# Performance work log

Hardware: AMD Instinct MI355X
Metric: run time of the kernel (lower is better)

The kernel has to match this reference:

```python
import jax, jax.numpy as jnp
import numpy as np

DIM = 2048        # model hidden size
INTER = 1408      # per-expert intermediate size
E = 16            # n_routed_experts
TOPK = 2          # n_activated_experts
S_INTER = 2816    # shared experts intermediate (n_shared_experts * INTER)
T = 4096          # tokens (batch*seq, module flattens to [-1, dim])
ROUTE_SCALE = 1.0


def setup_inputs() -> dict:
    key = jax.random.key(0)
    ks = jax.random.split(key, 8)
    g = lambda k, shape, scale: (jax.random.normal(k, shape, dtype=jnp.float32) * scale)
    return {
        "x": g(ks[0], (T, DIM), 1.0),
        "gate_w": g(ks[1], (E, DIM), 0.02),
        "w1": g(ks[2], (E, INTER, DIM), 0.02),
        "w2": g(ks[3], (E, DIM, INTER), 0.02),
        "w3": g(ks[4], (E, INTER, DIM), 0.02),
        "sw1": g(ks[5], (S_INTER, DIM), 0.02),
        "sw2": g(ks[6], (DIM, S_INTER), 0.02),
        "sw3": g(ks[7], (S_INTER, DIM), 0.02),
    }


def _moe_forward(x, gate_w, w1, w2, w3, sw1, sw2, sw3):
    t = x.shape[0]
    # ---- gate: softmax scores -> top-k experts per token ----
    scores = jax.nn.softmax(x @ gate_w.T, axis=-1)          # [T, E]
    top_w, top_i = jax.lax.top_k(scores, TOPK)              # [T, K]
    top_w = top_w * ROUTE_SCALE
    # dense combine weights [T, E]: zero for unselected experts
    combine = jnp.zeros((t, E), x.dtype).at[jnp.arange(t)[:, None], top_i].add(top_w)
    # ---- routed experts: gated silu MLP per expert, weighted combine ----
    # loop over the small fixed expert count; tokens with combine==0 contribute 0,
    # matching the original scatter/gather dispatch math exactly.
    y = jnp.zeros_like(x)
    for e in range(E):
        h = jax.nn.silu(x @ w1[e].T) * (x @ w3[e].T)        # [T, INTER]
        y = y + (h @ w2[e].T) * combine[:, e:e + 1]
    # ---- shared experts ----
    z = (jax.nn.silu(x @ sw1.T) * (x @ sw3.T)) @ sw2.T      # [T, DIM]
    return y + z


def reference(x, gate_w, w1, w2, w3, sw1, sw2, sw3):
    return _moe_forward(x, gate_w, w1, w2, w3, sw1, sw2, sw3)
```

## Files before the change

### kernel.cpp

```cpp
#include <hip/hip_runtime.h>
#include <hip/hip_bf16.h>
#include <cstdint>
#include <cstddef>

#define TTOK   4096
#define DIM_   2048
#define INTER_ 1408
#define NEXP   16
#define SINTER_ 2816
#define BM 128
#define BN 128
#define BK 64
#define MAXROWS (TTOK*2 + NEXP*BM)
#define MAXMT   (TTOK*2/BM + NEXP)

typedef unsigned short u16;
typedef __attribute__((ext_vector_type(8))) short short8;
typedef __attribute__((ext_vector_type(4))) float f32x4;

#define AS3P(p) ((__attribute__((address_space(3))) void*)(p))
#define AS1P(p) ((const __attribute__((address_space(1))) void*)(p))

__device__ __forceinline__ void gll16(const void* g, void* l) {
    __builtin_amdgcn_global_load_lds(AS1P(g), AS3P(l), 16, 0, 0);
}

__device__ __forceinline__ u16 f2bf(float f) {
    __hip_bfloat16 h = __float2bfloat16(f);
    union { __hip_bfloat16 h; u16 u; } c; c.h = h; return c.u;
}

__device__ __forceinline__ unsigned pk2(float a, float b) {
    unsigned r;
    asm("v_cvt_pk_bf16_f32 %0, %1, %2" : "=v"(r) : "v"(a), "v"(b));
    return r;
}

__device__ __forceinline__ int4 pack8(float4 a, float4 b) {
    int4 r;
    r.x = (int)pk2(a.x, a.y);
    r.y = (int)pk2(a.z, a.w);
    r.z = (int)pk2(b.x, b.y);
    r.w = (int)pk2(b.z, b.w);
    return r;
}


__global__ void init_kernel(int* perm_rt, float* pw_rt, int* misc, int* zrow) {
    int i = blockIdx.x * 256 + threadIdx.x;
    if (i < MAXROWS) { perm_rt[i] = -1; pw_rt[i] = 0.f; }
    if (i < 32)      misc[i] = 0;
    if (i < 1024)    zrow[i] = 0;
}

#define NW8  ((long)NEXP * INTER_ * DIM_ / 8)
#define NSW8 ((long)SINTER_ * DIM_ / 8)
#define NX8  ((long)TTOK * DIM_ / 8)
#define TOT8 (3 * NW8 + 3 * NSW8 + NX8)

__global__ void cvt_all_kernel(
    const float* __restrict__ w1, const float* __restrict__ w2,
    const float* __restrict__ w3, const float* __restrict__ sw1,
    const float* __restrict__ sw2, const float* __restrict__ sw3,
    const float* __restrict__ x,
    u16* __restrict__ w1b, u16* __restrict__ w2b, u16* __restrict__ w3b,
    u16* __restrict__ sw1b, u16* __restrict__ sw2b, u16* __restrict__ sw3b,
    u16* __restrict__ xb)
{
    const long stride = (long)gridDim.x * 256;
    for (long i = (long)blockIdx.x * 256 + threadIdx.x; i < TOT8; i += stride) {
        const float* s; u16* d; long off;
        if      (i <     NW8)              { s = w1;  d = w1b;  off = i; }
        else if (i < 2 * NW8)              { s = w2;  d = w2b;  off = i - NW8; }
        else if (i < 3 * NW8)              { s = w3;  d = w3b;  off = i - 2 * NW8; }
        else if (i < 3 * NW8 + NSW8)       { s = sw1; d = sw1b; off = i - 3 * NW8; }
        else if (i < 3 * NW8 + 2 * NSW8)   { s = sw2; d = sw2b; off = i - 3 * NW8 - NSW8; }
        else if (i < 3 * NW8 + 3 * NSW8)   { s = sw3; d = sw3b; off = i - 3 * NW8 - 2 * NSW8; }
        else                               { s = x;   d = xb;   off = i - 3 * NW8 - 3 * NSW8; }
        const float4* s4 = (const float4*)(s + off * 8);
        float4 a = s4[0], b = s4[1];
        *(int4*)(d + off * 8) = pack8(a, b);
    }
}

__global__ void gate_kernel(const float* __restrict__ x, const float* __restrict__ gw,
                            int* __restrict__ topi, float* __restrict__ topw,
                            int* __restrict__ misc) {
    int t = blockIdx.x;
    int lane = threadIdx.x;
    const float* xr = x + (size_t)t * DIM_;
    float acc[NEXP];
#pragma unroll
    for (int e = 0; e < NEXP; e++) acc[e] = 0.f;
#pragma unroll
    for (int i = 0; i < 8; i++) {
        int k = i * 256 + lane * 4;
        float4 xv = *(const float4*)(xr + k);
#pragma unroll
        for (int e = 0; e < NEXP; e++) {
            float4 gv = *(const float4*)(gw + (size_t)e * DIM_ + k);
            acc[e] += xv.x * gv.x + xv.y * gv.y + xv.z * gv.z + xv.w * gv.w;
        }
    }
#pragma unroll
    for (int e = 0; e < NEXP; e++) {
        float v = acc[e];
        for (int off = 32; off > 0; off >>= 1) v += __shfl_down(v, off);
        acc[e] = v;
    }
    if (lane == 0) {
        float m = acc[0];
#pragma unroll
        for (int e = 1; e < NEXP; e++) m = fmaxf(m, acc[e]);
        float p[NEXP]; float s = 0.f;
#pragma unroll
        for (int e = 0; e < NEXP; e++) { p[e] = __expf(acc[e] - m); s += p[e]; }
        int i0 = 0; float v0 = p[0];
#pragma unroll
        for (int e = 1; e < NEXP; e++) if (p[e] > v0) { v0 = p[e]; i0 = e; }
        int i1 = -1; float v1 = -1.f;
#pragma unroll
        for (int e = 0; e < NEXP; e++) if (e != i0 && p[e] > v1) { v1 = p[e]; i1 = e; }
        float inv = 1.f / s;
        topi[2 * t] = i0; topi[2 * t + 1] = i1;
        topw[2 * t] = v0 * inv; topw[2 * t + 1] = v1 * inv;
        atomicAdd(&misc[i0], 1);
        atomicAdd(&misc[i1], 1);
    }
}

__global__ void scan_kernel(int* misc) {
    int* counts = misc;
    int* base   = misc + 32;
    int* te     = misc + 48;
    int* tr     = misc + 128;
    int b = 0, tt = 0;
    for (int e = 0; e < NEXP; e++) {
        int c = counts[e];
        int nt = (c + BM - 1) >> 7;
        base[e] = b;
        for (int i = 0; i < nt; i++) { te[tt] = e; tr[tt] = b + i * BM; tt++; }
        b += nt * BM;
    }
    for (int i = tt; i < MAXMT; i++) te[i] = -1;
}

__global__ void scatter_kernel(const int* __restrict__ topi, const float* __restrict__ topw,
                               int* __restrict__ misc, int* __restrict__ perm,
                               float* __restrict__ pw) {
    int t = blockIdx.x * 256 + threadIdx.x;
    if (t >= TTOK) return;
    int* fill = misc + 16;
    int* base = misc + 32;
#pragma unroll
    for (int k = 0; k < 2; k++) {
        int e = topi[2 * t + k];
        int pos = base[e] + atomicAdd(&fill[e], 1);
        perm[pos] = t;
        pw[pos] = topw[2 * t + k];
    }
}


template<bool GROUPED>
__global__ __launch_bounds__(256, 2) void gemm_h13_k(
    const u16* __restrict__ Xb,
    const u16* __restrict__ W1b, const u16* __restrict__ W3b,
    u16* __restrict__ H,
    const int* __restrict__ perm,
    const int* __restrict__ te, const int* __restrict__ tr,
    const u16* __restrict__ zrow,
    int N, int K, int nt_m, int chunk)
{
    const int q = (blockIdx.x & 7) * chunk + (blockIdx.x >> 3);
    if (q >= nt_m * (N / BN)) return;
    const int jn = q / nt_m, im = q % nt_m;
    int e, slot0;
    if (GROUPED) { e = te[im]; if (e < 0) return; slot0 = tr[im]; }
    else         { e = 0; slot0 = im * BM; }
    const int n0 = jn * BN;
    const u16* W1 = W1b + (size_t)e * N * K;
    const u16* W3 = W3b + (size_t)e * N * K;

    __shared__ __align__(16) u16 As[BM * BK];
    __shared__ __align__(16) u16 B1s[BM * BK];
    __shared__ __align__(16) u16 B3s[BM * BK];

    const int tid = threadIdx.x;
    const int lane = tid & 63, wid = tid >> 6;
    const int wr = wid >> 1, wc = wid & 1;
    const int col = lane & 15, kg = lane >> 4;

    const int lr8 = lane >> 3;
    const int kb  = ((lane & 7) ^ lr8) * 8;
    const int rB0 = wid * 32 + lr8;
    const u16* gA[4];
#pragma unroll
    for (int i = 0; i < 4; i++) {
        if (GROUPED) {
            int ta = perm[slot0 + rB0 + 8 * i];
            gA[i] = (ta >= 0 ? Xb + (size_t)ta * K : zrow) + kb;
        } else {
            gA[i] = Xb + (size_t)(slot0 + rB0 + 8 * i) * K + kb;
        }
    }
    const u16* g1 = W1 + (size_t)(n0 + rB0) * K + kb;
    const u16* g3 = W3 + (size_t)(n0 + rB0) * K + kb;

    const int ldsI = (wid * 32) * BK;
    const int swr = col & 7;

    f32x4 acc1[4][4] = {};
    f32x4 acc3[4][4] = {};

    for (int k0 = 0; k0 < K; k0 += BK) {
#pragma unroll
        for (int i = 0; i < 4; i++) {
            gll16(gA[i] + k0, As + ldsI + i * 8 * BK);
            gll16(g1 + (size_t)(8 * i) * K + k0, B1s + ldsI + i * 8 * BK);
            gll16(g3 + (size_t)(8 * i) * K + k0, B3s + ldsI + i * 8 * BK);
        }
        __syncthreads();

        short8 a[4][2];
#pragma unroll
        for (int mi = 0; mi < 4; mi++)
#pragma unroll
            for (int t = 0; t < 2; t++) {
                int cc = kg + 4 * t;
                a[mi][t] = *(const short8*)(As + (wr * 64 + mi * 16 + col) * BK + ((cc ^ swr) * 8));
            }
#pragma unroll
        for (int t = 0; t < 2; t++) {
#pragma unroll
            for (int ni = 0; ni < 4; ni++) {
                int cc = kg + 4 * t;
                int off = (wc * 64 + ni * 16 + col) * BK + ((cc ^ swr) * 8);
                short8 v1 = *(const short8*)(B1s + off);
                short8 v3 = *(const short8*)(B3s + off);
#pragma unroll
                for (int mi = 0; mi < 4; mi++) {
                    acc1[mi][ni] = __builtin_amdgcn_mfma_f32_16x16x32_bf16(a[mi][t], v1, acc1[mi][ni], 0, 0, 0);
                    acc3[mi][ni] = __builtin_amdgcn_mfma_f32_16x16x32_bf16(a[mi][t], v3, acc3[mi][ni], 0, 0, 0);
                }
            }
        }
        __syncthreads();
    }

#pragma unroll
    for (int mi = 0; mi < 4; mi++) {
#pragma unroll
        for (int j = 0; j < 4; j++) {
            int row = slot0 + wr * 64 + mi * 16 + kg * 4 + j;
#pragma unroll
            for (int ni = 0; ni < 4; ni++) {
                float v1 = acc1[mi][ni][j];
                float v3 = acc3[mi][ni][j];
                float hv = v1 / (1.f + __expf(-v1)) * v3;
                int c = n0 + wc * 64 + ni * 16 + col;
                H[(size_t)row * N + c] = f2bf(hv);
            }
        }
    }
}


template<bool ATOMIC>
__global__ __launch_bounds__(256, 3) void gemm_out_k(
    const u16* __restrict__ Hm,
    const u16* __restrict__ W2b,
    float* __restrict__ Out,
    const int* __restrict__ perm, const float* __restrict__ pw,
    const int* __restrict__ te, const int* __restrict__ tr,
    int K, int nt_m, int chunk)
{
    const int q = (blockIdx.x & 7) * chunk + (blockIdx.x >> 3);
    if (q >= nt_m * (DIM_ / BN)) return;
    const int jn = q / nt_m, im = q % nt_m;
    int e, slot0;
    if (ATOMIC) { e = te[im]; if (e < 0) return; slot0 = tr[im]; }
    else        { e = 0; slot0 = im * BM; }
    const int n0 = jn * BN;
    const u16* W2 = W2b + (size_t)e * DIM_ * K;

    __shared__ __align__(16) u16 As[BM * BK];
    __shared__ __align__(16) u16 Bs[BM * BK];

    const int tid = threadIdx.x;
    const int lane = tid & 63, wid = tid >> 6;
    const int wr = wid >> 1, wc = wid & 1;
    const int col = lane & 15, kg = lane >> 4;

    const int lr8 = lane >> 3;
    const int kb  = ((lane & 7) ^ lr8) * 8;
    const int rB0 = wid * 32 + lr8;
    const u16* gA = Hm + (size_t)(slot0 + rB0) * K + kb;
    const u16* gB = W2 + (size_t)(n0 + rB0) * K + kb;
    const int ldsI = (wid * 32) * BK;
    const int swr = col & 7;

    f32x4 acc[4][4] = {};

    for (int k0 = 0; k0 < K; k0 += BK) {
#pragma unroll
        for (int i = 0; i < 4; i++) {
            gll16(gA + (size_t)(8 * i) * K + k0, As + ldsI + i * 8 * BK);
            gll16(gB + (size_t)(8 * i) * K + k0, Bs + ldsI + i * 8 * BK);
        }
        __syncthreads();

        short8 a[4][2];
#pragma unroll
        for (int mi = 0; mi < 4; mi++)
#pragma unroll
            for (int t = 0; t < 2; t++) {
                int cc = kg + 4 * t;
                a[mi][t] = *(const short8*)(As + (wr * 64 + mi * 16 + col) * BK + ((cc ^ swr) * 8));
            }
#pragma unroll
        for (int t = 0; t < 2; t++) {
#pragma unroll
            for (int ni = 0; ni < 4; ni++) {
                int cc = kg + 4 * t;
                int off = (wc * 64 + ni * 16 + col) * BK + ((cc ^ swr) * 8);
                short8 bv = *(const short8*)(Bs + off);
#pragma unroll
                for (int mi = 0; mi < 4; mi++)
                    acc[mi][ni] = __builtin_amdgcn_mfma_f32_16x16x32_bf16(a[mi][t], bv, acc[mi][ni], 0, 0, 0);
            }
        }
        __syncthreads();
    }

#pragma unroll
    for (int mi = 0; mi < 4; mi++) {
#pragma unroll
        for (int j = 0; j < 4; j++) {
            int rloc = wr * 64 + mi * 16 + kg * 4 + j;
            int slot = slot0 + rloc;
            if (ATOMIC) {
                int token = perm[slot];
                if (token < 0) continue;
                float w = pw[slot];
#pragma unroll
                for (int ni = 0; ni < 4; ni++) {
                    int c = n0 + wc * 64 + ni * 16 + col;
                    atomicAdd(&Out[(size_t)token * DIM_ + c], acc[mi][ni][j] * w);
                }
            } else {
#pragma unroll
                for (int ni = 0; ni < 4; ni++) {
                    int c = n0 + wc * 64 + ni * 16 + col;
                    Out[(size_t)slot * DIM_ + c] = acc[mi][ni][j];
                }
            }
        }
    }
}


extern "C" void kernel_launch(void* const* d_in, const int* in_sizes, int n_in,
                              void* d_out, int out_size, void* d_ws, size_t ws_size,
                              hipStream_t stream) {
    (void)in_sizes; (void)n_in; (void)out_size; (void)ws_size;
    const float* x   = (const float*)d_in[0];
    const float* gw  = (const float*)d_in[1];
    const float* w1  = (const float*)d_in[2];
    const float* w2  = (const float*)d_in[3];
    const float* w3  = (const float*)d_in[4];
    const float* sw1 = (const float*)d_in[5];
    const float* sw2 = (const float*)d_in[6];
    const float* sw3 = (const float*)d_in[7];
    float* out = (float*)d_out;

    char* ws = (char*)d_ws;
    size_t off = 0;
    auto take = [&](size_t bytes) -> void* {
        void* p = ws + off;
        off += (bytes + 255) & ~(size_t)255;
        return p;
    };
    const size_t nHB = ((size_t)MAXROWS * INTER_ > (size_t)TTOK * SINTER_)
                       ? (size_t)MAXROWS * INTER_ : (size_t)TTOK * SINTER_;
    u16*   xb      = (u16*)take((size_t)TTOK * DIM_ * 2);
    u16*   hbuf    = (u16*)take(nHB * 2);
    int*   perm_rt = (int*)take((size_t)MAXROWS * 4);
    float* pw_rt   = (float*)take((size_t)MAXROWS * 4);
    int*   topi    = (int*)take((size_t)TTOK * 2 * 4);
    float* topw    = (float*)take((size_t)TTOK * 2 * 4);
    int*   misc    = (int*)take(1024);
    int*   zrow    = (int*)take(4096);
    const size_t nW  = (size_t)NEXP * INTER_ * DIM_;
    const size_t nSW = (size_t)SINTER_ * DIM_;
    u16* w1b  = (u16*)take(nW * 2);
    u16* w2b  = (u16*)take(nW * 2);
    u16* w3b  = (u16*)take(nW * 2);
    u16* sw1b = (u16*)take(nSW * 2);
    u16* sw2b = (u16*)take(nSW * 2);
    u16* sw3b = (u16*)take(nSW * 2);

    init_kernel<<<MAXROWS / 256, 256, 0, stream>>>(perm_rt, pw_rt, misc, zrow);
    cvt_all_kernel<<<4096, 256, 0, stream>>>(w1, w2, w3, sw1, sw2, sw3, x,
                                             w1b, w2b, w3b, sw1b, sw2b, sw3b, xb);
    gate_kernel<<<TTOK, 64, 0, stream>>>(x, gw, topi, topw, misc);
    scan_kernel<<<1, 1, 0, stream>>>(misc);
    scatter_kernel<<<TTOK / 256, 256, 0, stream>>>(topi, topw, misc, perm_rt, pw_rt);

    auto grid8 = [](int total) { return ((total + 7) / 8) * 8; };
    auto chunk8 = [](int total) { return (total + 7) / 8; };

    const int ntm_sh = TTOK / BM;

    {
        int total = ntm_sh * (SINTER_ / BN);
        gemm_h13_k<false><<<grid8(total), 256, 0, stream>>>(
            xb, sw1b, sw3b, hbuf, nullptr, nullptr, nullptr, (const u16*)zrow,
            SINTER_, DIM_, ntm_sh, chunk8(total));
    }
    {
        int total = ntm_sh * (DIM_ / BN);
        gemm_out_k<false><<<grid8(total), 256, 0, stream>>>(
            hbuf, sw2b, out, nullptr, nullptr, nullptr, nullptr,
            SINTER_, ntm_sh, chunk8(total));
    }
    {
        int total = MAXMT * (INTER_ / BN);
        gemm_h13_k<true><<<grid8(total), 256, 0, stream>>>(
            xb, w1b, w3b, hbuf, perm_rt, misc + 48, misc + 128, (const u16*)zrow,
            INTER_, DIM_, MAXMT, chunk8(total));
    }
    {
        int total = MAXMT * (DIM_ / BN);
        gemm_out_k<true><<<grid8(total), 256, 0, stream>>>(
            hbuf, w2b, out, perm_rt, pw_rt, misc + 48, misc + 128,
            INTER_, MAXMT, chunk8(total));
    }
}
```

Baseline: 818.8 us.

## Double-buffer LDS tiles with async prefetch in both MoE GEMM kernels

Replaces the single-buffer BK=64 load/sync/compute loop with two LDS buffers of K-depth 32, issuing global_load_lds for the tile two steps ahead and waiting with explicit vmcnt counts plus barriers. Global-to-LDS latency can then overlap with MFMA work instead of stalling at each __syncthreads. The swizzle is redone for 32-wide rows, and the down-projection kernel's occupancy hint rises from 3 to 4 blocks. Each step now does half the MFMA work per barrier, so barrier overhead per FLOP goes up, and the hand-written waitcnt values must match the number of loads in flight.

After: 875.1 us. 6.9% more time.

```diff
diff --git a/kernel.cpp b/kernel.cpp
--- a/kernel.cpp
+++ b/kernel.cpp
@@ -10,7 +10,7 @@
 #define SINTER_ 2816
 #define BM 128
 #define BN 128
-#define BK 64
+#define HK 32
 #define MAXROWS (TTOK*2 + NEXP*BM)
 #define MAXMT   (TTOK*2/BM + NEXP)
 
@@ -44,6 +44,17 @@
     r.w = (int)pk2(b.z, b.w);
     return r;
 }
+
+#define PWAIT(NLIT) do { \
+    asm volatile("s_waitcnt vmcnt(" #NLIT ")" ::: "memory"); \
+    __builtin_amdgcn_s_barrier(); \
+    asm volatile("" ::: "memory"); \
+} while (0)
+#define PDONE() do { \
+    asm volatile("" ::: "memory"); \
+    __builtin_amdgcn_s_barrier(); \
+    asm volatile("" ::: "memory"); \
+} while (0)
 
 
 __global__ void init_kernel(int* perm_rt, float* pw_rt, int* misc, int* zrow) {
@@ -182,70 +193,82 @@
     const u16* W1 = W1b + (size_t)e * N * K;
     const u16* W3 = W3b + (size_t)e * N * K;
 
-    __shared__ __align__(16) u16 As[BM * BK];
-    __shared__ __align__(16) u16 B1s[BM * BK];
-    __shared__ __align__(16) u16 B3s[BM * BK];
+    __shared__ __align__(16) u16 As[2][BM * HK];
+    __shared__ __align__(16) u16 B1s[2][BM * HK];
+    __shared__ __align__(16) u16 B3s[2][BM * HK];
 
     const int tid = threadIdx.x;
     const int lane = tid & 63, wid = tid >> 6;
     const int wr = wid >> 1, wc = wid & 1;
     const int col = lane & 15, kg = lane >> 4;
 
-    const int lr8 = lane >> 3;
-    const int kb  = ((lane & 7) ^ lr8) * 8;
-    const int rB0 = wid * 32 + lr8;
-    const u16* gA[4];
-#pragma unroll
-    for (int i = 0; i < 4; i++) {
-        if (GROUPED) {
-            int ta = perm[slot0 + rB0 + 8 * i];
-            gA[i] = (ta >= 0 ? Xb + (size_t)ta * K : zrow) + kb;
-        } else {
-            gA[i] = Xb + (size_t)(slot0 + rB0 + 8 * i) * K + kb;
-        }
-    }
-    const u16* g1 = W1 + (size_t)(n0 + rB0) * K + kb;
-    const u16* g3 = W3 + (size_t)(n0 + rB0) * K + kb;
-
-    const int ldsI = (wid * 32) * BK;
-    const int swr = col & 7;
+    const int lr = lane >> 2;
+    const int kb = ((lane & 3) ^ ((lane >> 3) & 3)) * 8;
+    const int ar0 = wid * 32 + lr, ar1 = ar0 + 16;
+    const u16* ga0;
+    const u16* ga1;
+    if (GROUPED) {
+        const int ta0 = perm[slot0 + ar0];
+        const int ta1 = perm[slot0 + ar1];
+        ga0 = (ta0 >= 0 ? Xb + (size_t)ta0 * K : zrow) + kb;
+        ga1 = (ta1 >= 0 ? Xb + (size_t)ta1 * K : zrow) + kb;
+    } else {
+        ga0 = Xb + (size_t)(slot0 + ar0) * K + kb;
+        ga1 = Xb + (size_t)(slot0 + ar1) * K + kb;
+    }
+    const u16* gb1a = W1 + (size_t)(n0 + ar0) * K + kb;
+    const u16* gb1b = W1 + (size_t)(n0 + ar1) * K + kb;
+    const u16* gb3a = W3 + (size_t)(n0 + ar0) * K + kb;
+    const u16* gb3b = W3 + (size_t)(n0 + ar1) * K + kb;
+    const int lo0 = (wid * 32) * HK;
+    const int lo1 = (wid * 32 + 16) * HK;
+
+    const int sw = (col >> 1) & 3;
 
     f32x4 acc1[4][4] = {};
     f32x4 acc3[4][4] = {};
 
-    for (int k0 = 0; k0 < K; k0 += BK) {
-#pragma unroll
-        for (int i = 0; i < 4; i++) {
-            gll16(gA[i] + k0, As + ldsI + i * 8 * BK);
-            gll16(g1 + (size_t)(8 * i) * K + k0, B1s + ldsI + i * 8 * BK);
-            gll16(g3 + (size_t)(8 * i) * K + k0, B3s + ldsI + i * 8 * BK);
-        }
-        __syncthreads();
-
-        short8 a[4][2];
+    auto ISSUE = [&](int h) {
+        const int b = h & 1;
+        const int ko = h * HK;
+        gll16(ga0 + ko, &As[b][lo0]);
+        gll16(ga1 + ko, &As[b][lo1]);
+        gll16(gb1a + ko, &B1s[b][lo0]);
+        gll16(gb1b + ko, &B1s[b][lo1]);
+        gll16(gb3a + ko, &B3s[b][lo0]);
+        gll16(gb3b + ko, &B3s[b][lo1]);
+    };
+
+    const int nh = K / HK;
+    ISSUE(0);
+    ISSUE(1);
+
+    for (int h = 0; h < nh; ++h) {
+        if (h + 1 < nh) PWAIT(6); else PWAIT(0);
+
+        const int b = h & 1;
+        const u16* Ac  = As[b];
+        const u16* B1c = B1s[b];
+        const u16* B3c = B3s[b];
+
+        short8 a[4];
 #pragma unroll
         for (int mi = 0; mi < 4; mi++)
-#pragma unroll
-            for (int t = 0; t < 2; t++) {
-                int cc = kg + 4 * t;
-                a[mi][t] = *(const short8*)(As + (wr * 64 + mi * 16 + col) * BK + ((cc ^ swr) * 8));
-            }
-#pragma unroll
-        for (int t = 0; t < 2; t++) {
-#pragma unroll
-            for (int ni = 0; ni < 4; ni++) {
-                int cc = kg + 4 * t;
-                int off = (wc * 64 + ni * 16 + col) * BK + ((cc ^ swr) * 8);
-                short8 v1 = *(const short8*)(B1s + off);
-                short8 v3 = *(const short8*)(B3s + off);
-#pragma unroll
-                for (int mi = 0; mi < 4; mi++) {
-                    acc1[mi][ni] = __builtin_amdgcn_mfma_f32_16x16x32_bf16(a[mi][t], v1, acc1[mi][ni], 0, 0, 0);
-                    acc3[mi][ni] = __builtin_amdgcn_mfma_f32_16x16x32_bf16(a[mi][t], v3, acc3[mi][ni], 0, 0, 0);
-                }
+            a[mi] = *(const short8*)(Ac + (wr * 64 + mi * 16 + col) * HK + ((kg ^ sw) * 8));
+#pragma unroll
+        for (int ni = 0; ni < 4; ni++) {
+            const int off = (wc * 64 + ni * 16 + col) * HK + ((kg ^ sw) * 8);
+            short8 v1 = *(const short8*)(B1c + off);
+            short8 v3 = *(const short8*)(B3c + off);
+#pragma unroll
+            for (int mi = 0; mi < 4; mi++) {
+                acc1[mi][ni] = __builtin_amdgcn_mfma_f32_16x16x32_bf16(a[mi], v1, acc1[mi][ni], 0, 0, 0);
+                acc3[mi][ni] = __builtin_amdgcn_mfma_f32_16x16x32_bf16(a[mi], v3, acc3[mi][ni], 0, 0, 0);
             }
         }
-        __syncthreads();
+
+        PDONE();
+        if (h + 2 < nh) ISSUE(h + 2);
     }
 
 #pragma unroll
@@ -267,7 +290,7 @@
 
 
 template<bool ATOMIC>
-__global__ __launch_bounds__(256, 3) void gemm_out_k(
+__global__ __launch_bounds__(256, 4) void gemm_out_k(
     const u16* __restrict__ Hm,
     const u16* __restrict__ W2b,
     float* __restrict__ Out,
@@ -284,53 +307,62 @@
     const int n0 = jn * BN;
     const u16* W2 = W2b + (size_t)e * DIM_ * K;
 
-    __shared__ __align__(16) u16 As[BM * BK];
-    __shared__ __align__(16) u16 Bs[BM * BK];
+    __shared__ __align__(16) u16 As[2][BM * HK];
+    __shared__ __align__(16) u16 Bs[2][BM * HK];
 
     const int tid = threadIdx.x;
     const int lane = tid & 63, wid = tid >> 6;
     const int wr = wid >> 1, wc = wid & 1;
     const int col = lane & 15, kg = lane >> 4;
 
-    const int lr8 = lane >> 3;
-    const int kb  = ((lane & 7) ^ lr8) * 8;
-    const int rB0 = wid * 32 + lr8;
-    const u16* gA = Hm + (size_t)(slot0 + rB0) * K + kb;
-    const u16* gB = W2 + (size_t)(n0 + rB0) * K + kb;
-    const int ldsI = (wid * 32) * BK;
-    const int swr = col & 7;
+    const int lr = lane >> 2;
+    const int kb = ((lane & 3) ^ ((lane >> 3) & 3)) * 8;
+    const int ar0 = wid * 32 + lr, ar1 = ar0 + 16;
+    const u16* ga0 = Hm + (size_t)(slot0 + ar0) * K + kb;
+    const u16* ga1 = Hm + (size_t)(slot0 + ar1) * K + kb;
+    const u16* gb0 = W2 + (size_t)(n0 + ar0) * K + kb;
+    const u16* gb1 = W2 + (size_t)(n0 + ar1) * K + kb;
+    const int lo0 = (wid * 32) * HK;
+    const int lo1 = (wid * 32 + 16) * HK;
+
+    const int sw = (col >> 1) & 3;
 
     f32x4 acc[4][4] = {};
 
-    for (int k0 = 0; k0 < K; k0 += BK) {
-#pragma unroll
-        for (int i = 0; i < 4; i++) {
-            gll16(gA + (size_t)(8 * i) * K + k0, As + ldsI + i * 8 * BK);
-            gll16(gB + (size_t)(8 * i) * K + k0, Bs + ldsI + i * 8 * BK);
+    auto ISSUE = [&](int h) {
+        const int b = h & 1;
+        const int ko = h * HK;
+        gll16(ga0 + ko, &As[b][lo0]);
+        gll16(ga1 + ko, &As[b][lo1]);
+        gll16(gb0 + ko, &Bs[b][lo0]);
+        gll16(gb1 + ko, &Bs[b][lo1]);
+    };
+
+    const int nh = K / HK;
+    ISSUE(0);
+    ISSUE(1);
+
+    for (int h = 0; h < nh; ++h) {
+        if (h + 1 < nh) PWAIT(4); else PWAIT(0);
+
+        const int b = h & 1;
+        const u16* Ac = As[b];
+        const u16* Bc = Bs[b];
+
+        short8 a[4];
+#pragma unroll
+        for (int mi = 0; mi < 4; mi++)
+            a[mi] = *(const short8*)(Ac + (wr * 64 + mi * 16 + col) * HK + ((kg ^ sw) * 8));
+#pragma unroll
+        for (int ni = 0; ni < 4; ni++) {
+            short8 bv = *(const short8*)(Bc + (wc * 64 + ni * 16 + col) * HK + ((kg ^ sw) * 8));
+#pragma unroll
+            for (int mi = 0; mi < 4; mi++)
+                acc[mi][ni] = __builtin_amdgcn_mfma_f32_16x16x32_bf16(a[mi], bv, acc[mi][ni], 0, 0, 0);
         }
-        __syncthreads();
-
-        short8 a[4][2];
-#pragma unroll
-        for (int mi = 0; mi < 4; mi++)
-#pragma unroll
-            for (int t = 0; t < 2; t++) {
-                int cc = kg + 4 * t;
-                a[mi][t] = *(const short8*)(As + (wr * 64 + mi * 16 + col) * BK + ((cc ^ swr) * 8));
-            }
-#pragma unroll
-        for (int t = 0; t < 2; t++) {
-#pragma unroll
-            for (int ni = 0; ni < 4; ni++) {
-                int cc = kg + 4 * t;
-                int off = (wc * 64 + ni * 16 + col) * BK + ((cc ^ swr) * 8);
-                short8 bv = *(const short8*)(Bs + off);
-#pragma unroll
-                for (int mi = 0; mi < 4; mi++)
-                    acc[mi][ni] = __builtin_amdgcn_mfma_f32_16x16x32_bf16(a[mi][t], bv, acc[mi][ni], 0, 0, 0);
-            }
-        }
-        __syncthreads();
+
+        PDONE();
+        if (h + 2 < nh) ISSUE(h + 2);
     }
 
 #pragma unroll
```

## Merge shared and routed expert GEMMs into single launches per stage

Applied to the files above, without the earlier changes.

Folds the shared-expert GEMMs into the routed-expert GEMM launches, so one kernel computes both H stages and one kernel computes both output projections. Shared weights are laid out right after the routed weights so a single base pointer plus offset addresses either. Output is zeroed inside the conversion kernel, which also absorbs the separate init kernel. Every output write now goes through an atomic add, and the larger grids are meant to fill the device better and cut launch gaps and tail effects. The cost is extra atomic traffic for the shared-expert outputs.

After: 818.8 us. No clear change (-0.0%).

```diff
diff --git a/kernel.cpp b/kernel.cpp
--- a/kernel.cpp
+++ b/kernel.cpp
@@ -14,6 +14,13 @@
 #define MAXROWS (TTOK*2 + NEXP*BM)
 #define MAXMT   (TTOK*2/BM + NEXP)
 
+#define NT_SH_H  ((TTOK/BM) * (SINTER_/BN))
+#define NT_RT_H  (MAXMT * (INTER_/BN))
+#define NT_H     (NT_SH_H + NT_RT_H)
+#define NT_SH_O  ((TTOK/BM) * (DIM_/BN))
+#define NT_RT_O  (MAXMT * (DIM_/BN))
+#define NT_O     (NT_SH_O + NT_RT_O)
+
 typedef unsigned short u16;
 typedef __attribute__((ext_vector_type(8))) short short8;
 typedef __attribute__((ext_vector_type(4))) float f32x4;
@@ -45,14 +52,6 @@
     return r;
 }
 
-
-__global__ void init_kernel(int* perm_rt, float* pw_rt, int* misc, int* zrow) {
-    int i = blockIdx.x * 256 + threadIdx.x;
-    if (i < MAXROWS) { perm_rt[i] = -1; pw_rt[i] = 0.f; }
-    if (i < 32)      misc[i] = 0;
-    if (i < 1024)    zrow[i] = 0;
-}
-
 #define NW8  ((long)NEXP * INTER_ * DIM_ / 8)
 #define NSW8 ((long)SINTER_ * DIM_ / 8)
 #define NX8  ((long)TTOK * DIM_ / 8)
@@ -65,10 +64,21 @@
     const float* __restrict__ x,
     u16* __restrict__ w1b, u16* __restrict__ w2b, u16* __restrict__ w3b,
     u16* __restrict__ sw1b, u16* __restrict__ sw2b, u16* __restrict__ sw3b,
-    u16* __restrict__ xb)
+    u16* __restrict__ xb,
+    int* __restrict__ perm_rt, float* __restrict__ pw_rt,
+    int* __restrict__ misc, int* __restrict__ zrow,
+    float* __restrict__ outz)
 {
     const long stride = (long)gridDim.x * 256;
-    for (long i = (long)blockIdx.x * 256 + threadIdx.x; i < TOT8; i += stride) {
+    const long gid = (long)blockIdx.x * 256 + threadIdx.x;
+
+    if (gid < MAXROWS) { perm_rt[gid] = -1; pw_rt[gid] = 0.f; }
+    if (gid < 32)      misc[gid] = 0;
+    if (gid < 1024)    zrow[gid] = 0;
+    for (long i = gid; i < (long)TTOK * DIM_ / 4; i += stride)
+        *(float4*)(outz + i * 4) = make_float4(0.f, 0.f, 0.f, 0.f);
+
+    for (long i = gid; i < TOT8; i += stride) {
         const float* s; u16* d; long off;
         if      (i <     NW8)              { s = w1;  d = w1b;  off = i; }
         else if (i < 2 * NW8)              { s = w2;  d = w2b;  off = i - NW8; }
@@ -162,25 +172,32 @@
 }
 
 
-template<bool GROUPED>
-__global__ __launch_bounds__(256, 2) void gemm_h13_k(
+__global__ __launch_bounds__(256, 2) void gemm_h13_m(
     const u16* __restrict__ Xb,
     const u16* __restrict__ W1b, const u16* __restrict__ W3b,
-    u16* __restrict__ H,
+    u16* __restrict__ HS, u16* __restrict__ HR,
     const int* __restrict__ perm,
     const int* __restrict__ te, const int* __restrict__ tr,
     const u16* __restrict__ zrow,
-    int N, int K, int nt_m, int chunk)
+    int K, int chunk)
 {
     const int q = (blockIdx.x & 7) * chunk + (blockIdx.x >> 3);
-    if (q >= nt_m * (N / BN)) return;
-    const int jn = q / nt_m, im = q % nt_m;
-    int e, slot0;
-    if (GROUPED) { e = te[im]; if (e < 0) return; slot0 = tr[im]; }
-    else         { e = 0; slot0 = im * BM; }
+    if (q >= NT_H) return;
+    int im, jn, N, slot0; size_t eoff; u16* H; bool gather;
+    if (q < NT_SH_H) {
+        im = q % (TTOK / BM); jn = q / (TTOK / BM);
+        N = SINTER_; slot0 = im * BM; eoff = (size_t)NEXP * INTER_ * DIM_;
+        H = HS; gather = false;
+    } else {
+        int q2 = q - NT_SH_H;
+        im = q2 % MAXMT; jn = q2 / MAXMT;
+        int e = te[im]; if (e < 0) return;
+        slot0 = tr[im]; N = INTER_; eoff = (size_t)e * INTER_ * DIM_;
+        H = HR; gather = true;
+    }
     const int n0 = jn * BN;
-    const u16* W1 = W1b + (size_t)e * N * K;
-    const u16* W3 = W3b + (size_t)e * N * K;
+    const u16* W1 = W1b + eoff;
+    const u16* W3 = W3b + eoff;
 
     __shared__ __align__(16) u16 As[BM * BK];
     __shared__ __align__(16) u16 B1s[BM * BK];
@@ -197,11 +214,12 @@
     const u16* gA[4];
 #pragma unroll
     for (int i = 0; i < 4; i++) {
-        if (GROUPED) {
-            int ta = perm[slot0 + rB0 + 8 * i];
+        int row = slot0 + rB0 + 8 * i;
+        if (gather) {
+            int ta = perm[row];
             gA[i] = (ta >= 0 ? Xb + (size_t)ta * K : zrow) + kb;
         } else {
-            gA[i] = Xb + (size_t)(slot0 + rB0 + 8 * i) * K + kb;
+            gA[i] = Xb + (size_t)row * K + kb;
         }
     }
     const u16* g1 = W1 + (size_t)(n0 + rB0) * K + kb;
@@ -266,23 +284,30 @@
 }
 
 
-template<bool ATOMIC>
-__global__ __launch_bounds__(256, 3) void gemm_out_k(
-    const u16* __restrict__ Hm,
+__global__ __launch_bounds__(256, 3) void gemm_out_m(
+    const u16* __restrict__ HS, const u16* __restrict__ HR,
     const u16* __restrict__ W2b,
     float* __restrict__ Out,
     const int* __restrict__ perm, const float* __restrict__ pw,
     const int* __restrict__ te, const int* __restrict__ tr,
-    int K, int nt_m, int chunk)
+    int chunk)
 {
     const int q = (blockIdx.x & 7) * chunk + (blockIdx.x >> 3);
-    if (q >= nt_m * (DIM_ / BN)) return;
-    const int jn = q / nt_m, im = q % nt_m;
-    int e, slot0;
-    if (ATOMIC) { e = te[im]; if (e < 0) return; slot0 = tr[im]; }
-    else        { e = 0; slot0 = im * BM; }
+    if (q >= NT_O) return;
+    int im, jn, K, slot0; size_t eoff; const u16* A; bool gather;
+    if (q < NT_SH_O) {
+        im = q % (TTOK / BM); jn = q / (TTOK / BM);
+        K = SINTER_; slot0 = im * BM; eoff = (size_t)NEXP * INTER_ * DIM_;
+        A = HS; gather = false;
+    } else {
+        int q2 = q - NT_SH_O;
+        im = q2 % MAXMT; jn = q2 / MAXMT;
+        int e = te[im]; if (e < 0) return;
+        slot0 = tr[im]; K = INTER_; eoff = (size_t)e * INTER_ * DIM_;
+        A = HR; gather = true;
+    }
     const int n0 = jn * BN;
-    const u16* W2 = W2b + (size_t)e * DIM_ * K;
+    const u16* W2 = W2b + eoff;
 
     __shared__ __align__(16) u16 As[BM * BK];
     __shared__ __align__(16) u16 Bs[BM * BK];
@@ -295,7 +320,7 @@
     const int lr8 = lane >> 3;
     const int kb  = ((lane & 7) ^ lr8) * 8;
     const int rB0 = wid * 32 + lr8;
-    const u16* gA = Hm + (size_t)(slot0 + rB0) * K + kb;
+    const u16* gA = A + (size_t)(slot0 + rB0) * K + kb;
     const u16* gB = W2 + (size_t)(n0 + rB0) * K + kb;
     const int ldsI = (wid * 32) * BK;
     const int swr = col & 7;
@@ -339,21 +364,19 @@
         for (int j = 0; j < 4; j++) {
             int rloc = wr * 64 + mi * 16 + kg * 4 + j;
             int slot = slot0 + rloc;
-            if (ATOMIC) {
-                int token = perm[slot];
+            int token; float w;
+            if (gather) {
+                token = perm[slot];
                 if (token < 0) continue;
-                float w = pw[slot];
-#pragma unroll
-                for (int ni = 0; ni < 4; ni++) {
-                    int c = n0 + wc * 64 + ni * 16 + col;
-                    atomicAdd(&Out[(size_t)token * DIM_ + c], acc[mi][ni][j] * w);
-                }
+                w = pw[slot];
             } else {
-#pragma unroll
-                for (int ni = 0; ni < 4; ni++) {
-                    int c = n0 + wc * 64 + ni * 16 + col;
-                    Out[(size_t)slot * DIM_ + c] = acc[mi][ni][j];
-                }
+                token = slot;
+                w = 1.f;
+            }
+#pragma unroll
+            for (int ni = 0; ni < 4; ni++) {
+                int c = n0 + wc * 64 + ni * 16 + col;
+                atomicAdd(&Out[(size_t)token * DIM_ + c], acc[mi][ni][j] * w);
             }
         }
     }
@@ -381,10 +404,9 @@
         off += (bytes + 255) & ~(size_t)255;
         return p;
     };
-    const size_t nHB = ((size_t)MAXROWS * INTER_ > (size_t)TTOK * SINTER_)
-                       ? (size_t)MAXROWS * INTER_ : (size_t)TTOK * SINTER_;
     u16*   xb      = (u16*)take((size_t)TTOK * DIM_ * 2);
-    u16*   hbuf    = (u16*)take(nHB * 2);
+    u16*   hbufS   = (u16*)take((size_t)TTOK * SINTER_ * 2);
+    u16*   hbufR   = (u16*)take((size_t)MAXROWS * INTER_ * 2);
     int*   perm_rt = (int*)take((size_t)MAXROWS * 4);
     float* pw_rt   = (float*)take((size_t)MAXROWS * 4);
     int*   topi    = (int*)take((size_t)TTOK * 2 * 4);
@@ -394,46 +416,24 @@
     const size_t nW  = (size_t)NEXP * INTER_ * DIM_;
     const size_t nSW = (size_t)SINTER_ * DIM_;
     u16* w1b  = (u16*)take(nW * 2);
+    u16* sw1b = (u16*)take(nSW * 2);
+    u16* w3b  = (u16*)take(nW * 2);
+    u16* sw3b = (u16*)take(nSW * 2);
     u16* w2b  = (u16*)take(nW * 2);
-    u16* w3b  = (u16*)take(nW * 2);
-    u16* sw1b = (u16*)take(nSW * 2);
     u16* sw2b = (u16*)take(nSW * 2);
-    u16* sw3b = (u16*)take(nSW * 2);
-
-    init_kernel<<<MAXROWS / 256, 256, 0, stream>>>(perm_rt, pw_rt, misc, zrow);
+
     cvt_all_kernel<<<4096, 256, 0, stream>>>(w1, w2, w3, sw1, sw2, sw3, x,
-                                             w1b, w2b, w3b, sw1b, sw2b, sw3b, xb);
+                                             w1b, w2b, w3b, sw1b, sw2b, sw3b, xb,
+                                             perm_rt, pw_rt, misc, zrow, out);
     gate_kernel<<<TTOK, 64, 0, stream>>>(x, gw, topi, topw, misc);
     scan_kernel<<<1, 1, 0, stream>>>(misc);
     scatter_kernel<<<TTOK / 256, 256, 0, stream>>>(topi, topw, misc, perm_rt, pw_rt);
 
-    auto grid8 = [](int total) { return ((total + 7) / 8) * 8; };
-    auto chunk8 = [](int total) { return (total + 7) / 8; };
-
-    const int ntm_sh = TTOK / BM;
-
-    {
-        int total = ntm_sh * (SINTER_ / BN);
-        gemm_h13_k<false><<<grid8(total), 256, 0, stream>>>(
-            xb, sw1b, sw3b, hbuf, nullptr, nullptr, nullptr, (const u16*)zrow,
-            SINTER_, DIM_, ntm_sh, chunk8(total));
-    }
-    {
-        int total = ntm_sh * (DIM_ / BN);
-        gemm_out_k<false><<<grid8(total), 256, 0, stream>>>(
-            hbuf, sw2b, out, nullptr, nullptr, nullptr, nullptr,
-            SINTER_, ntm_sh, chunk8(total));
-    }
-    {
-        int total = MAXMT * (INTER_ / BN);
-        gemm_h13_k<true><<<grid8(total), 256, 0, stream>>>(
-            xb, w1b, w3b, hbuf, perm_rt, misc + 48, misc + 128, (const u16*)zrow,
-            INTER_, DIM_, MAXMT, chunk8(total));
-    }
-    {
-        int total = MAXMT * (DIM_ / BN);
-        gemm_out_k<true><<<grid8(total), 256, 0, stream>>>(
-            hbuf, w2b, out, perm_rt, pw_rt, misc + 48, misc + 128,
-            INTER_, MAXMT, chunk8(total));
-    }
-}
+    gemm_h13_m<<<NT_H, 256, 0, stream>>>(
+        xb, w1b, w3b, hbufS, hbufR, perm_rt, misc + 48, misc + 128,
+        (const u16*)zrow, DIM_, NT_H / 8);
+
+    gemm_out_m<<<NT_O, 256, 0, stream>>>(
+        hbufS, hbufR, w2b, out, perm_rt, pw_rt, misc + 48, misc + 128,
+        NT_O / 8);
+}
```
